# Kernel optimization log

Hardware: AMD Instinct MI355X
Metric: run time of the kernel (lower is better)

The kernel has to match this reference:

```python
import jax, jax.numpy as jnp
import numpy as np
import math

D_MODEL = 1024
NUM_HEADS = 16
D_HEAD = 64
K_EIG = 16
B, N = 4, 4096


def setup_inputs() -> dict:
    key = jax.random.key(0)
    ks = jax.random.split(key, 8)
    s = 1.0 / math.sqrt(D_MODEL)
    return {
        "x": jax.random.normal(ks[0], (B, N, D_MODEL), jnp.float32),
        "Wq": jax.random.normal(ks[1], (D_MODEL, NUM_HEADS * D_HEAD), jnp.float32) * s,
        "bq": jnp.zeros((NUM_HEADS * D_HEAD,), jnp.float32),
        "Wk": jax.random.normal(ks[2], (D_MODEL, NUM_HEADS * D_HEAD), jnp.float32) * s,
        "bk": jnp.zeros((NUM_HEADS * D_HEAD,), jnp.float32),
        "Wv": jax.random.normal(ks[3], (D_MODEL, NUM_HEADS * D_HEAD), jnp.float32) * s,
        "bv": jnp.zeros((NUM_HEADS * D_HEAD,), jnp.float32),
        "eigenvectors": jax.random.normal(ks[4], (NUM_HEADS, K_EIG), jnp.float32),
        "filter_weights": jnp.ones((K_EIG,), jnp.float32),
    }


def reference(x, Wq, bq, Wk, bk, Wv, bv, eigenvectors, filter_weights):
    Bb, Nn, _ = x.shape
    H, Dh = NUM_HEADS, D_HEAD
    # projections -> [B,N,H,Dh]
    Q = (x @ Wq + bq).reshape(Bb, Nn, H, Dh)
    K = (x @ Wk + bk).reshape(Bb, Nn, H, Dh)
    V = (x @ Wv + bv).reshape(Bb, Nn, H, Dh)
    # head axis -> eigen (frequency) axis: [B,N,K,Dh]
    Qf = jnp.einsum('hk,bnhd->bnkd', eigenvectors, Q)
    Kf = jnp.einsum('hk,bnhd->bnkd', eigenvectors, K)
    Vf = jnp.einsum('hk,bnhd->bnkd', eigenvectors, V)
    # learnable spectral filter, broadcast over eigen axis
    w = filter_weights[None, None, :, None]
    Qf = Qf * w
    Kf = Kf * w
    Vf = Vf * w
    # small k x k attention per token
    scores = jnp.einsum('bnkd,bnld->bnkl', Qf, Kf) / math.sqrt(Dh)
    attn = jax.nn.softmax(scores, axis=-1)  # dropout is identity in eval
    out_f = jnp.einsum('bnkl,bnld->bnkd', attn, Vf)
    # back to head space: [B,N,H,Dh]
    out = jnp.einsum('hk,bnkd->bnhd', eigenvectors, out_f)
    return out.reshape(Bb, Nn, H * Dh)
```

## Files before the change

kernel.cpp:

```cpp
#include <hip/hip_runtime.h>
#include <stdint.h>

#define NTOK   16384
#define DM     1024
#define NQKV   3072

typedef __attribute__((ext_vector_type(8))) _Float16 half8;
typedef __attribute__((ext_vector_type(4))) _Float16 half4;
typedef __attribute__((ext_vector_type(4))) float    float4v;

__device__ __forceinline__ void async_cp16(const void* g, void* l){
  __builtin_amdgcn_global_load_lds(
      (const __attribute__((address_space(1))) void*)g,
      (__attribute__((address_space(3))) void*)l, 16, 0, 0);
}

__global__ void cvt_x_kernel(const float* __restrict__ x, _Float16* __restrict__ xb){
  int i = (blockIdx.x * blockDim.x + threadIdx.x) * 8;
  const int stride = gridDim.x * blockDim.x * 8;
  for(; i < NTOK * DM; i += stride){
    float4v v0 = *(const float4v*)(x + i);
    float4v v1 = *(const float4v*)(x + i + 4);
    half8 o;
    o[0]=(_Float16)v0[0]; o[1]=(_Float16)v0[1]; o[2]=(_Float16)v0[2]; o[3]=(_Float16)v0[3];
    o[4]=(_Float16)v1[0]; o[5]=(_Float16)v1[1]; o[6]=(_Float16)v1[2]; o[7]=(_Float16)v1[3];
    *(half8*)(xb + i) = o;
  }
}

__global__ __launch_bounds__(256)
void prep_w_kernel(const float* __restrict__ Wq, const float* __restrict__ Wk,
                   const float* __restrict__ Wv, const float* __restrict__ E,
                   const float* __restrict__ fw, _Float16* __restrict__ WT){
  __shared__ float Wl[8][1032];
  __shared__ float oT[16][8][65];
  __shared__ float sEv[256];
  __shared__ float sFw[16];
  const int t  = threadIdx.x;
  const int bx = blockIdx.x;
  const int p  = bx >> 7, rt = bx & 127;
  const int c0 = rt * 8;
  const float* W = (p == 0) ? Wq : (p == 1) ? Wk : Wv;
  sEv[t] = E[t];
  if(t < 16) sFw[t] = fw[t];

  #pragma unroll
  for(int j = 0; j < 32; ++j){
    const int flat = j * 256 + t;
    const int row = flat >> 10, col = flat & 1023;
    Wl[row][col] = W[(size_t)(c0 + row) * 1024 + col];
  }
  __syncthreads();

  const int d = t & 63, rg = t >> 6;
  #pragma unroll
  for(int rr = 0; rr < 2; ++rr){
    const int row = rg * 2 + rr;
    float w[16];
    #pragma unroll
    for(int h = 0; h < 16; ++h) w[h] = Wl[row][h * 64 + d];
    #pragma unroll
    for(int ke = 0; ke < 16; ++ke){
      float acc = 0.f;
      #pragma unroll
      for(int h = 0; h < 16; ++h) acc += sEv[h * 16 + ke] * w[h];
      oT[ke][row][d] = acc * sFw[ke];
    }
  }
  __syncthreads();

  #pragma unroll
  for(int k4 = 0; k4 < 4; ++k4){
    const int idx = k4 * 256 + t;
    const int ke = idx >> 6, dd = idx & 63;
    half8 o;
    #pragma unroll
    for(int c = 0; c < 8; ++c) o[c] = (_Float16)oT[ke][c][dd];
    const int n = (p * 16 + ke) * 64 + dd;
    *(half8*)(WT + (size_t)n * 1024 + c0) = o;
  }
}

__global__ void prep_b_kernel(const float* __restrict__ bq, const float* __restrict__ bk,
                              const float* __restrict__ bv, const float* __restrict__ E,
                              const float* __restrict__ fw, float* __restrict__ fb){
  const int n = blockIdx.x * blockDim.x + threadIdx.x;
  if(n >= NQKV) return;
  const int p = n >> 10, kE = (n >> 6) & 15, d = n & 63;
  const float* b = (p == 0) ? bq : (p == 1) ? bk : bv;
  float acc = 0.f;
  for(int h = 0; h < 16; ++h) acc += E[h * 16 + kE] * b[h * 64 + d];
  fb[n] = acc * fw[kE];
}

__global__ __launch_bounds__(256)
void gemm_qkv_kernel(const _Float16* __restrict__ A,
                     const _Float16* __restrict__ BT,
                     const float* __restrict__ bias,
                     _Float16* __restrict__ C){
  __shared__ _Float16 As[128 * 32];
  __shared__ _Float16 Bs[128 * 32];
  const int t = threadIdx.x;
  const int lane = t & 63, wv = t >> 6;
  const int l15 = lane & 15, q = lane >> 4;
  const int l = blockIdx.x + blockIdx.y * 24;
  const int xcd = l & 7, s = l >> 3;
  const int m0 = (xcd * 16 + (s & 15)) * 128;
  const int n0 = (s >> 4) * 128;
  const int wm = (wv & 1) * 64, wn = (wv >> 1) * 64;

  float4v acc[4][4];
  #pragma unroll
  for(int i = 0; i < 4; ++i)
    #pragma unroll
    for(int j = 0; j < 4; ++j){ acc[i][j][0]=0.f; acc[i][j][1]=0.f; acc[i][j][2]=0.f; acc[i][j][3]=0.f; }

  const int ar = t >> 2;
  const int ac = (t & 3) * 8;
  const _Float16* ga0 = A  + (size_t)(m0 + ar)      * 1024 + ac;
  const _Float16* ga1 = A  + (size_t)(m0 + 64 + ar) * 1024 + ac;
  const _Float16* gb0 = BT + (size_t)(n0 + ar)      * 1024 + ac;
  const _Float16* gb1 = BT + (size_t)(n0 + 64 + ar) * 1024 + ac;

  for(int k0 = 0; k0 < 1024; k0 += 32){
    async_cp16(ga0 + k0, As + t * 8);
    async_cp16(ga1 + k0, As + 2048 + t * 8);
    async_cp16(gb0 + k0, Bs + t * 8);
    async_cp16(gb1 + k0, Bs + 2048 + t * 8);
    __syncthreads();
    half8 af[4], bf[4];
    #pragma unroll
    for(int i = 0; i < 4; ++i) af[i] = *(const half8*)(As + (wm + i * 16 + l15) * 32 + q * 8);
    #pragma unroll
    for(int j = 0; j < 4; ++j) bf[j] = *(const half8*)(Bs + (wn + j * 16 + l15) * 32 + q * 8);
    #pragma unroll
    for(int i = 0; i < 4; ++i)
      #pragma unroll
      for(int j = 0; j < 4; ++j)
        acc[i][j] = __builtin_amdgcn_mfma_f32_16x16x32_f16(af[i], bf[j], acc[i][j], 0, 0, 0);
    __syncthreads();
  }
  #pragma unroll
  for(int j = 0; j < 4; ++j){
    const int n = n0 + wn + j * 16 + l15;
    const float bs = bias[n];
    #pragma unroll
    for(int i = 0; i < 4; ++i){
      const int mg = m0 + wm + i * 16 + q * 4;
      #pragma unroll
      for(int r = 0; r < 4; ++r)
        C[(size_t)(mg + r) * NQKV + n] = (_Float16)(acc[i][j][r] + bs);
    }
  }
}

__global__ __launch_bounds__(256)
void attn_kernel(const _Float16* __restrict__ QKV,
                 const float* __restrict__ E,
                 float* __restrict__ out){
  __shared__ _Float16 sV[4 * 1024];
  __shared__ _Float16 sE[16 * 32];
  __shared__ _Float16 pT[4][16 * 32];
  __shared__ _Float16 gT[4][16 * 32];

  const int t = threadIdx.x, lane = t & 63, wv = t >> 6;
  const int l15 = lane & 15, q = lane >> 4;

  {
    #pragma unroll
    for(int s = 0; s < 2; ++s){
      const int idx = s * 256 + t;
      const int row = idx >> 5, col = idx & 31;
      sE[idx] = (col < 16) ? (_Float16)E[row * 16 + col] : (_Float16)0.f;
    }
    #pragma unroll
    for(int s = 0; s < 4; ++s){
      const int idx = s * 256 + t;
      const int w = idx >> 8, rem = idx & 255;
      const int off = (rem >> 4) * 32 + 16 + (rem & 15);
      pT[w][off] = (_Float16)0.f;
      gT[w][off] = (_Float16)0.f;
    }
  }

  const _Float16* gb = QKV + (size_t)blockIdx.x * (4 * 3072);
  #pragma unroll
  for(int i = 0; i < 2; ++i){
    const int f = i * 256 + t;
    async_cp16(gb + (f >> 7) * 3072 + 2048 + (f & 127) * 8, sV + f * 8);
  }

  const int tok = blockIdx.x * 4 + wv;
  const _Float16* tg = QKV + (size_t)tok * 3072;

  half8 aK0 = *(const half8*)(tg + 1024 + l15 * 64 + q * 8);
  half8 aK1 = *(const half8*)(tg + 1024 + l15 * 64 + 32 + q * 8);
  half8 bQ0 = *(const half8*)(tg + l15 * 64 + q * 8);
  half8 bQ1 = *(const half8*)(tg + l15 * 64 + 32 + q * 8);
  float4v S; S[0]=0.f; S[1]=0.f; S[2]=0.f; S[3]=0.f;
  S = __builtin_amdgcn_mfma_f32_16x16x32_f16(aK0, bQ0, S, 0, 0, 0);
  S = __builtin_amdgcn_mfma_f32_16x16x32_f16(aK1, bQ1, S, 0, 0, 0);

  float v[4];
  #pragma unroll
  for(int r = 0; r < 4; ++r) v[r] = S[r] * 0.125f;
  float mx = fmaxf(fmaxf(v[0], v[1]), fmaxf(v[2], v[3]));
  mx = fmaxf(mx, __shfl_xor(mx, 16));
  mx = fmaxf(mx, __shfl_xor(mx, 32));
  float e[4];
  #pragma unroll
  for(int r = 0; r < 4; ++r) e[r] = __expf(v[r] - mx);
  float sm = (e[0] + e[1]) + (e[2] + e[3]);
  sm += __shfl_xor(sm, 16);
  sm += __shfl_xor(sm, 32);
  const float rs = 1.f / sm;

  __syncthreads();

  _Float16* pw = pT[wv];
  #pragma unroll
  for(int r = 0; r < 4; ++r) pw[(q * 4 + r) * 32 + l15] = (_Float16)(e[r] * rs);
  half8 bP = *(const half8*)(pw + l15 * 32 + q * 8);
  half8 aE = *(const half8*)(sE + l15 * 32 + q * 8);

  float4v G; G[0]=0.f; G[1]=0.f; G[2]=0.f; G[3]=0.f;
  G = __builtin_amdgcn_mfma_f32_16x16x32_f16(aE, bP, G, 0, 0, 0);

  _Float16* gw = gT[wv];
  #pragma unroll
  for(int r = 0; r < 4; ++r) gw[(q * 4 + r) * 32 + l15] = (_Float16)G[r];
  half8 aG = *(const half8*)(gw + l15 * 32 + q * 8);

  const _Float16* vb = sV + wv * 1024 + (q & 1) * 8 * 64;
  float* ob = out + (size_t)tok * 1024;
  #pragma unroll
  for(int tt = 0; tt < 4; ++tt){
    half8 vf;
    #pragma unroll
    for(int jj = 0; jj < 8; ++jj) vf[jj] = vb[jj * 64 + tt * 16 + l15];
    float4v O; O[0]=0.f; O[1]=0.f; O[2]=0.f; O[3]=0.f;
    O = __builtin_amdgcn_mfma_f32_16x16x32_f16(aG, vf, O, 0, 0, 0);
    #pragma unroll
    for(int r = 0; r < 4; ++r)
      ob[(q * 4 + r) * 64 + tt * 16 + l15] = O[r];
  }
}

extern "C" void kernel_launch(void* const* d_in, const int* in_sizes, int n_in,
                              void* d_out, int out_size, void* d_ws, size_t ws_size,
                              hipStream_t stream){
  const float* x  = (const float*)d_in[0];
  const float* Wq = (const float*)d_in[1];
  const float* bq = (const float*)d_in[2];
  const float* Wk = (const float*)d_in[3];
  const float* bk = (const float*)d_in[4];
  const float* Wv = (const float*)d_in[5];
  const float* bv = (const float*)d_in[6];
  const float* E  = (const float*)d_in[7];
  const float* fw = (const float*)d_in[8];
  float* out = (float*)d_out;

  char* ws = (char*)d_ws;
  _Float16* xb  = (_Float16*)ws;
  _Float16* WT  = (_Float16*)(ws + (size_t)32 * 1024 * 1024);
  float*    fb  = (float*)   (ws + (size_t)39 * 1024 * 1024);
  _Float16* QKV = (_Float16*)(ws + (size_t)40 * 1024 * 1024);

  hipLaunchKernelGGL(cvt_x_kernel, dim3(2048), dim3(256), 0, stream, x, xb);
  hipLaunchKernelGGL(prep_w_kernel, dim3(384), dim3(256), 0, stream, Wq, Wk, Wv, E, fw, WT);
  hipLaunchKernelGGL(prep_b_kernel, dim3(12), dim3(256), 0, stream, bq, bk, bv, E, fw, fb);
  hipLaunchKernelGGL(gemm_qkv_kernel, dim3(24, 128), dim3(256), 0, stream, xb, WT, fb, QKV);
  hipLaunchKernelGGL(attn_kernel, dim3(NTOK / 4), dim3(256), 0, stream, QKV, E, out);
}
```

Measured before the change: 310.9 us.

## Rewrite QKV GEMM as 256x256 double-buffered, swizzled, 8-wave pipelined kernel

Replaces the 128x128, single-buffered QKV GEMM (BK=32, two barriers per step) with a 256x256 tile, BK=64 kernel using 8 waves and 128 KB of dynamic LDS for double buffering. Loads for the next k-tile are issued in four chunks interleaved with four MFMA quadrants, with explicit vmcnt/lgkmcnt waits, raw barriers and s_setprio. The LDS layout is XOR-swizzled to avoid bank conflicts. This targets global-load latency and LDS stalls at the cost of larger register and LDS use, which limits occupancy, and of much finer synchronisation that is harder to get right.

```diff
diff --git a/kernel.cpp b/kernel.cpp
--- a/kernel.cpp
+++ b/kernel.cpp
@@ -8,6 +8,11 @@
 typedef __attribute__((ext_vector_type(8))) _Float16 half8;
 typedef __attribute__((ext_vector_type(4))) _Float16 half4;
 typedef __attribute__((ext_vector_type(4))) float    float4v;
+
+#define MFMA16 __builtin_amdgcn_mfma_f32_16x16x32_f16
+#define BARX()  do{ asm volatile("" ::: "memory"); __builtin_amdgcn_s_barrier(); asm volatile("" ::: "memory"); }while(0)
+#define LGKM0() asm volatile("s_waitcnt lgkmcnt(0)" ::: "memory")
+#define VMCNT(N) asm volatile("s_waitcnt vmcnt(" #N ")" ::: "memory")
 
 __device__ __forceinline__ void async_cp16(const void* g, void* l){
   __builtin_amdgcn_global_load_lds(
@@ -93,63 +98,158 @@
   fb[n] = acc * fw[kE];
 }
 
-__global__ __launch_bounds__(256)
+struct FlagF { static constexpr bool value = false; };
+struct FlagT { static constexpr bool value = true; };
+
+__global__ __launch_bounds__(512, 2)
 void gemm_qkv_kernel(const _Float16* __restrict__ A,
                      const _Float16* __restrict__ BT,
                      const float* __restrict__ bias,
                      _Float16* __restrict__ C){
-  __shared__ _Float16 As[128 * 32];
-  __shared__ _Float16 Bs[128 * 32];
+  extern __shared__ _Float16 lds[];
   const int t = threadIdx.x;
   const int lane = t & 63, wv = t >> 6;
   const int l15 = lane & 15, q = lane >> 4;
-  const int l = blockIdx.x + blockIdx.y * 24;
-  const int xcd = l & 7, s = l >> 3;
-  const int m0 = (xcd * 16 + (s & 15)) * 128;
-  const int n0 = (s >> 4) * 128;
-  const int wm = (wv & 1) * 64, wn = (wv >> 1) * 64;
-
-  float4v acc[4][4];
-  #pragma unroll
-  for(int i = 0; i < 4; ++i)
-    #pragma unroll
-    for(int j = 0; j < 4; ++j){ acc[i][j][0]=0.f; acc[i][j][1]=0.f; acc[i][j][2]=0.f; acc[i][j][3]=0.f; }
-
-  const int ar = t >> 2;
-  const int ac = (t & 3) * 8;
-  const _Float16* ga0 = A  + (size_t)(m0 + ar)      * 1024 + ac;
-  const _Float16* ga1 = A  + (size_t)(m0 + 64 + ar) * 1024 + ac;
-  const _Float16* gb0 = BT + (size_t)(n0 + ar)      * 1024 + ac;
-  const _Float16* gb1 = BT + (size_t)(n0 + 64 + ar) * 1024 + ac;
-
-  for(int k0 = 0; k0 < 1024; k0 += 32){
-    async_cp16(ga0 + k0, As + t * 8);
-    async_cp16(ga1 + k0, As + 2048 + t * 8);
-    async_cp16(gb0 + k0, Bs + t * 8);
-    async_cp16(gb1 + k0, Bs + 2048 + t * 8);
-    __syncthreads();
-    half8 af[4], bf[4];
-    #pragma unroll
-    for(int i = 0; i < 4; ++i) af[i] = *(const half8*)(As + (wm + i * 16 + l15) * 32 + q * 8);
-    #pragma unroll
-    for(int j = 0; j < 4; ++j) bf[j] = *(const half8*)(Bs + (wn + j * 16 + l15) * 32 + q * 8);
-    #pragma unroll
-    for(int i = 0; i < 4; ++i)
-      #pragma unroll
-      for(int j = 0; j < 4; ++j)
-        acc[i][j] = __builtin_amdgcn_mfma_f32_16x16x32_f16(af[i], bf[j], acc[i][j], 0, 0, 0);
-    __syncthreads();
-  }
-  #pragma unroll
-  for(int j = 0; j < 4; ++j){
-    const int n = n0 + wn + j * 16 + l15;
-    const float bs = bias[n];
-    #pragma unroll
-    for(int i = 0; i < 4; ++i){
-      const int mg = m0 + wm + i * 16 + q * 4;
+  const int wr = wv >> 2, wc = wv & 3;
+
+  const int bid = blockIdx.x;
+  const int xcd = bid & 7, s = bid >> 3;
+  const int mt = xcd * 8 + (s & 7);
+  const int nt = s >> 3;
+  const int m0 = mt * 256, n0 = nt * 256;
+
+  const int stR = wv * 16 + (lane >> 3);
+  const int stC = (((lane & 7) ^ (lane >> 3)) * 8);
+  const int stD = (wv * 128 + lane) * 8;
+  const int qsw = (q * 8) ^ ((l15 & 7) * 8);
+  const int aoffb = (wr * 16 + l15) * 64;
+  const int boffb = (wc * 16 + l15) * 64;
+
+  auto stgA = [&](_Float16* nb, int kc, int h){
+    const _Float16* g = A + (size_t)(m0 + h * 128 + stR) * 1024 + kc + stC;
+    _Float16* d = nb + h * 8192 + stD;
+    async_cp16(g, d);
+    async_cp16(g + 8 * 1024, d + 512);
+  };
+  auto stgB = [&](_Float16* nb, int kc, int h){
+    const _Float16* g = BT + (size_t)(n0 + h * 128 + stR) * 1024 + kc + stC;
+    _Float16* d = nb + 16384 + h * 8192 + stD;
+    async_cp16(g, d);
+    async_cp16(g + 8 * 1024, d + 512);
+  };
+
+  float4v acc[8][4];
+  #pragma unroll
+  for(int m = 0; m < 8; ++m)
+    #pragma unroll
+    for(int n = 0; n < 4; ++n){ acc[m][n][0]=0.f; acc[m][n][1]=0.f; acc[m][n][2]=0.f; acc[m][n][3]=0.f; }
+
+  half8 aL[4][2], aH[4][2], b0[2][2], b1[2][2];
+
+  stgA(lds, 0, 0);
+  stgB(lds, 0, 0);
+  stgB(lds, 0, 1);
+  stgA(lds, 0, 1);
+  VMCNT(4);
+  BARX();
+
+  int kt = 0;
+  auto ktile = [&](auto lastc){
+    constexpr bool LAST = decltype(lastc)::value;
+    const _Float16* pA = lds + (kt & 1) * 32768;
+    const _Float16* pB = pA + 16384;
+    _Float16* nxt = lds + ((kt + 1) & 1) * 32768;
+    const int kn = (kt + 1) * 64;
+
+    #pragma unroll
+    for(int m = 0; m < 4; ++m){
+      aL[m][0] = *(const half8*)(pA + aoffb + m * 2048 + qsw);
+      aL[m][1] = *(const half8*)(pA + aoffb + m * 2048 + (qsw ^ 32));
+    }
+    #pragma unroll
+    for(int n = 0; n < 2; ++n){
+      b0[n][0] = *(const half8*)(pB + boffb + n * 4096 + qsw);
+      b0[n][1] = *(const half8*)(pB + boffb + n * 4096 + (qsw ^ 32));
+    }
+    if constexpr(!LAST) stgA(nxt, kn, 0);
+    BARX(); LGKM0();
+    __builtin_amdgcn_s_setprio(1);
+    #pragma unroll
+    for(int m = 0; m < 4; ++m)
+      #pragma unroll
+      for(int n = 0; n < 2; ++n){
+        acc[m][n] = MFMA16(aL[m][0], b0[n][0], acc[m][n], 0, 0, 0);
+        acc[m][n] = MFMA16(aL[m][1], b0[n][1], acc[m][n], 0, 0, 0);
+      }
+    __builtin_amdgcn_s_setprio(0);
+    if constexpr(!LAST){ VMCNT(4); } else { VMCNT(2); }
+    BARX();
+
+    #pragma unroll
+    for(int n = 0; n < 2; ++n){
+      b1[n][0] = *(const half8*)(pB + boffb + (n + 2) * 4096 + qsw);
+      b1[n][1] = *(const half8*)(pB + boffb + (n + 2) * 4096 + (qsw ^ 32));
+    }
+    if constexpr(!LAST) stgB(nxt, kn, 0);
+    BARX(); LGKM0();
+    __builtin_amdgcn_s_setprio(1);
+    #pragma unroll
+    for(int m = 0; m < 4; ++m)
+      #pragma unroll
+      for(int n = 0; n < 2; ++n){
+        acc[m][n + 2] = MFMA16(aL[m][0], b1[n][0], acc[m][n + 2], 0, 0, 0);
+        acc[m][n + 2] = MFMA16(aL[m][1], b1[n][1], acc[m][n + 2], 0, 0, 0);
+      }
+    __builtin_amdgcn_s_setprio(0);
+    if constexpr(!LAST){ VMCNT(4); } else { VMCNT(0); }
+    BARX();
+
+    #pragma unroll
+    for(int m = 0; m < 4; ++m){
+      aH[m][0] = *(const half8*)(pA + aoffb + (m + 4) * 2048 + qsw);
+      aH[m][1] = *(const half8*)(pA + aoffb + (m + 4) * 2048 + (qsw ^ 32));
+    }
+    if constexpr(!LAST) stgB(nxt, kn, 1);
+    BARX(); LGKM0();
+    __builtin_amdgcn_s_setprio(1);
+    #pragma unroll
+    for(int m = 0; m < 4; ++m)
+      #pragma unroll
+      for(int n = 0; n < 2; ++n){
+        acc[m + 4][n] = MFMA16(aH[m][0], b0[n][0], acc[m + 4][n], 0, 0, 0);
+        acc[m + 4][n] = MFMA16(aH[m][1], b0[n][1], acc[m + 4][n], 0, 0, 0);
+      }
+    __builtin_amdgcn_s_setprio(0);
+    BARX();
+
+    if constexpr(!LAST) stgA(nxt, kn, 1);
+    BARX(); LGKM0();
+    __builtin_amdgcn_s_setprio(1);
+    #pragma unroll
+    for(int m = 0; m < 4; ++m)
+      #pragma unroll
+      for(int n = 0; n < 2; ++n){
+        acc[m + 4][n + 2] = MFMA16(aH[m][0], b1[n][0], acc[m + 4][n + 2], 0, 0, 0);
+        acc[m + 4][n + 2] = MFMA16(aH[m][1], b1[n][1], acc[m + 4][n + 2], 0, 0, 0);
+      }
+    __builtin_amdgcn_s_setprio(0);
+    if constexpr(!LAST){ VMCNT(4); }
+    BARX();
+  };
+
+  for(kt = 0; kt < 15; ++kt) ktile(FlagF{});
+  ktile(FlagT{});
+
+  #pragma unroll
+  for(int n = 0; n < 4; ++n){
+    const int col = n0 + (n * 4 + wc) * 16 + l15;
+    const float bs = bias[col];
+    #pragma unroll
+    for(int m = 0; m < 8; ++m){
+      const int rbase = m0 + (m * 2 + wr) * 16 + q * 4;
       #pragma unroll
       for(int r = 0; r < 4; ++r)
-        C[(size_t)(mg + r) * NQKV + n] = (_Float16)(acc[i][j][r] + bs);
+        C[(size_t)(rbase + r) * NQKV + col] = (_Float16)(acc[m][n][r] + bs);
     }
   }
 }
@@ -266,9 +366,16 @@
   float*    fb  = (float*)   (ws + (size_t)39 * 1024 * 1024);
   _Float16* QKV = (_Float16*)(ws + (size_t)40 * 1024 * 1024);
 
+  static bool attr_done = false;
+  if(!attr_done){
+    hipFuncSetAttribute((const void*)gemm_qkv_kernel,
+                        hipFuncAttributeMaxDynamicSharedMemorySize, 131072);
+    attr_done = true;
+  }
+
   hipLaunchKernelGGL(cvt_x_kernel, dim3(2048), dim3(256), 0, stream, x, xb);
   hipLaunchKernelGGL(prep_w_kernel, dim3(384), dim3(256), 0, stream, Wq, Wk, Wv, E, fw, WT);
   hipLaunchKernelGGL(prep_b_kernel, dim3(12), dim3(256), 0, stream, bq, bk, bv, E, fw, fb);
-  hipLaunchKernelGGL(gemm_qkv_kernel, dim3(24, 128), dim3(256), 0, stream, xb, WT, fb, QKV);
+  hipLaunchKernelGGL(gemm_qkv_kernel, dim3(768), dim3(512), 131072, stream, xb, WT, fb, QKV);
   hipLaunchKernelGGL(attn_kernel, dim3(NTOK / 4), dim3(256), 0, stream, QKV, E, out);
 }
```

New measurement: 285.5 us. -8.2%, faster.
